# Kernel tuning notes

Measured on AMD Instinct MI355X. Metric: run time of the kernel, lower is better.

Reference implementation:

```python
import jax, jax.numpy as jnp
import numpy as np

B, S, D = 2, 2048, 2048
NH, NKV, HD = 32, 8, 64
RATIO = NH // NKV  # 4
EPS = 1e-6


def setup_inputs() -> dict:
    key = jax.random.key(0)
    ks = jax.random.split(key, 6)
    x = jax.random.normal(ks[0], (B, S, D), dtype=jnp.float32)
    # weights stored (in, out) so projection is x @ W
    wq = jax.random.normal(ks[1], (D, NH * HD), dtype=jnp.float32) * 0.02
    wk = jax.random.normal(ks[2], (D, NKV * HD), dtype=jnp.float32) * 0.02
    wv = jax.random.normal(ks[3], (D, NKV * HD), dtype=jnp.float32) * 0.02
    wo = jax.random.normal(ks[4], (NH * HD, D), dtype=jnp.float32) * 0.02
    q_scale = jnp.ones((HD,), dtype=jnp.float32)
    k_scale = jnp.ones((HD,), dtype=jnp.float32)
    # RoPE tables (S, HD): duplicated-half layout
    inv_freq = 1.0 / (10000.0 ** (np.arange(0, HD, 2, dtype=np.float32) / HD))
    t = np.arange(S, dtype=np.float32)
    freqs = np.outer(t, inv_freq)  # (S, HD/2)
    emb = np.concatenate([freqs, freqs], axis=-1)  # (S, HD)
    cos = jnp.asarray(np.cos(emb))
    sin = jnp.asarray(np.sin(emb))
    # causal mask: True above diagonal = masked
    mask = jnp.triu(jnp.ones((S, S), dtype=jnp.bool_), k=1)
    return {"x": x, "wq": wq, "wk": wk, "wv": wv, "wo": wo,
            "q_scale": q_scale, "k_scale": k_scale,
            "cos": cos, "sin": sin, "mask": mask}


def _rms_norm(x, scale):
    # Qwen3-compatible: compute in fp32, cast back
    idt = x.dtype
    xf = x.astype(jnp.float32)
    nx = xf * jax.lax.rsqrt(jnp.mean(xf * xf, axis=-1, keepdims=True) + EPS)
    return (nx * scale).astype(idt)


def _rope(x, cos, sin):
    # x: (b, h, s, hd); cos/sin: (s, hd)
    hd = x.shape[-1]
    x1, x2 = x[..., : hd // 2], x[..., hd // 2:]
    rot = jnp.concatenate([-x2, x1], axis=-1)
    return x * cos[None, None] + rot * sin[None, None]


def reference(x, wq, wk, wv, wo, q_scale, k_scale, cos, sin, mask):
    b, sl, _ = x.shape
    q = (x @ wq).reshape(b, sl, NH, HD).transpose(0, 2, 1, 3)    # (b, nh, s, hd)
    k = (x @ wk).reshape(b, sl, NKV, HD).transpose(0, 2, 1, 3)   # (b, nkv, s, hd)
    v = (x @ wv).reshape(b, sl, NKV, HD).transpose(0, 2, 1, 3)   # (b, nkv, s, hd)
    q = _rms_norm(q, q_scale)
    k = _rms_norm(k, k_scale)
    q = _rope(q, cos, sin)
    k = _rope(k, cos, sin)
    # GQA: repeat KV heads
    k = jnp.repeat(k, RATIO, axis=1)  # (b, nh, s, hd)
    v = jnp.repeat(v, RATIO, axis=1)
    scores = jnp.einsum('bhqd,bhkd->bhqk', q, k) / jnp.sqrt(jnp.float32(HD))
    scores = jnp.where(mask[None, None], jnp.finfo(scores.dtype).min, scores)
    attn = jax.nn.softmax(scores, axis=-1)
    out = jnp.einsum('bhqk,bhkd->bhqd', attn, v)
    out = out.transpose(0, 2, 1, 3).reshape(b, sl, NH * HD)
    return out @ wo
```

## Files before the change

### kernel.cpp

```cpp
#include <hip/hip_runtime.h>
#include <hip/hip_bf16.h>

typedef float f32x4 __attribute__((ext_vector_type(4)));
typedef float f32x16 __attribute__((ext_vector_type(16)));
typedef short s16x8 __attribute__((ext_vector_type(8)));
typedef unsigned short u16;
typedef unsigned short u16x8 __attribute__((ext_vector_type(8)));
typedef unsigned short u16x4 __attribute__((ext_vector_type(4)));
typedef unsigned int u32;
typedef unsigned int u32x4 __attribute__((ext_vector_type(4)));

#define MROWS 4096
#define NQKV  3072
#define DMODEL 2048

#define EXP2(x) __builtin_amdgcn_exp2f(x)

__device__ __forceinline__ u16 f2bf(float f) {
  __hip_bfloat16 h = __float2bfloat16(f);
  return __builtin_bit_cast(u16, h);
}
__device__ __forceinline__ float bf2f(u16 u) {
  __hip_bfloat16 h = __builtin_bit_cast(__hip_bfloat16, u);
  return __bfloat162float(h);
}

typedef __attribute__((address_space(3))) unsigned int lds_u32_t;
typedef const __attribute__((address_space(1))) unsigned int glb_u32_t;
__device__ __forceinline__ void gload_lds16(const void* g, void* l) {
  __builtin_amdgcn_global_load_lds((glb_u32_t*)g, (lds_u32_t*)l, 16, 0, 0);
}

__global__ __launch_bounds__(256) void k_conv_x(const float* __restrict__ x, u16* __restrict__ o) {
  size_t i = ((size_t)blockIdx.x * 256 + threadIdx.x) * 4;
  float4 v = *(const float4*)(x + i);
  u16x4 r = { f2bf(v.x), f2bf(v.y), f2bf(v.z), f2bf(v.w) };
  *(u16x4*)(o + i) = r;
}

__global__ __launch_bounds__(256) void k_transw(const float* __restrict__ src, u16* __restrict__ dst,
                                                int N, int K) {
  __shared__ u16 t[64][68];
  int n0 = blockIdx.x * 64, k0 = blockIdx.y * 64;
  int tid = threadIdx.x;
#pragma unroll
  for (int r = 0; r < 4; ++r) {
    int k = r * 16 + (tid >> 4);
    int n = (tid & 15) * 4;
    float4 v = *(const float4*)(src + (size_t)(k0 + k) * N + n0 + n);
    t[n + 0][k] = f2bf(v.x);
    t[n + 1][k] = f2bf(v.y);
    t[n + 2][k] = f2bf(v.z);
    t[n + 3][k] = f2bf(v.w);
  }
  __syncthreads();
#pragma unroll
  for (int r = 0; r < 4; ++r) {
    int n = r * 16 + (tid >> 4);
    int k = (tid & 15) * 4;
    u16x4 o = { t[n][k], t[n][k + 1], t[n][k + 2], t[n][k + 3] };
    *(u16x4*)(dst + (size_t)(n0 + n) * K + k0 + k) = o;
  }
}

template <int BM, int BN, typename OutT>
__global__ __launch_bounds__(512, 2)
void k_gemm8(const u16* __restrict__ A, const u16* __restrict__ Bt,
             OutT* __restrict__ C, int M, int N, int K, int nbx) {
  static_assert(BM == 128, "A staging assumes one full 512x16B round");
  constexpr int WM = 2, WN = 4;
  constexpr int MF = BM / 16 / WM;
  constexpr int NF = BN / 16 / WN;
  __shared__ u16 sA[2][2][BM][32];
  __shared__ u16 sB[2][2][BN][32];
  const int nwg = gridDim.x;
  const int chunk = nwg >> 3;
  const int wg = (blockIdx.x & 7) * chunk + (blockIdx.x >> 3);
  const int m0 = (wg / nbx) * BM, n0 = (wg % nbx) * BN;
  const int tid = threadIdx.x;
  const int l = tid & 63;
  const int lo = l & 15, hi = l >> 4;
  const int wid = tid >> 6;
  const int wm = wid >> 2, wn = wid & 3;
  const int nkt = K >> 6;

  f32x4 acc[MF][NF] = {};

  auto STAGE = [&](int buf, int ks, int t) {
    {
      const int D = tid * 16;
      const int row = D >> 6;
      const int srcb = (D & 63) ^ (((row >> 1) & 3) << 4);
      gload_lds16((const char*)(A + (size_t)(m0 + row) * K + t * 64 + ks * 32) + srcb,
                  (char*)(&sA[buf][ks][0][0]) + D);
    }
#pragma unroll
    for (int i = 0; i < 2; ++i) {
      const int u = i * 512 + tid;
      if ((BN * 4) % 512 == 0 || u < BN * 4) {
        const int D = u * 16;
        const int row = D >> 6;
        const int srcb = (D & 63) ^ (((row >> 1) & 3) << 4);
        gload_lds16((const char*)(Bt + (size_t)(n0 + row) * K + t * 64 + ks * 32) + srcb,
                    (char*)(&sB[buf][ks][0][0]) + D);
      }
    }
  };

  auto WAITVM = [&]() {
    if constexpr (BN == 192) {
      if (wid < 4) asm volatile("s_waitcnt vmcnt(3)" ::: "memory");
      else         asm volatile("s_waitcnt vmcnt(2)" ::: "memory");
    } else {
      asm volatile("s_waitcnt vmcnt(3)" ::: "memory");
    }
  };

  auto PHASE = [&](int buf, int ks, int t1, bool st, int vmmode) {
    s16x8 a[MF], b[NF];
#pragma unroll
    for (int mf = 0; mf < MF; ++mf) {
      const int row = wm * (MF * 16) + mf * 16 + lo;
      a[mf] = *(const s16x8*)((const char*)(&sA[buf][ks][0][0]) + row * 64 +
                              ((hi * 16) ^ (((row >> 1) & 3) << 4)));
    }
#pragma unroll
    for (int nf = 0; nf < NF; ++nf) {
      const int row = wn * (NF * 16) + nf * 16 + lo;
      b[nf] = *(const s16x8*)((const char*)(&sB[buf][ks][0][0]) + row * 64 +
                              ((hi * 16) ^ (((row >> 1) & 3) << 4)));
    }
    if (st) STAGE(buf ^ 1, ks, t1);
    __builtin_amdgcn_sched_barrier(0);
    __builtin_amdgcn_s_barrier();
    asm volatile("s_waitcnt lgkmcnt(0)" ::: "memory");
    __builtin_amdgcn_sched_barrier(0);
    __builtin_amdgcn_s_setprio(1);
#pragma unroll
    for (int mf = 0; mf < MF; ++mf)
#pragma unroll
      for (int nf = 0; nf < NF; ++nf)
        acc[mf][nf] = __builtin_amdgcn_mfma_f32_16x16x32_bf16(a[mf], b[nf], acc[mf][nf], 0, 0, 0);
    __builtin_amdgcn_s_setprio(0);
    if (vmmode == 1) WAITVM();
    else if (vmmode == 2) asm volatile("s_waitcnt vmcnt(0)" ::: "memory");
    __builtin_amdgcn_sched_barrier(0);
    __builtin_amdgcn_s_barrier();
  };

  STAGE(0, 0, 0);
  STAGE(0, 1, 0);
  WAITVM();
  __builtin_amdgcn_s_barrier();

  for (int t = 0; t < nkt; ++t) {
    const int buf = t & 1;
    const bool st = (t + 1 < nkt);
    PHASE(buf, 0, t + 1, st, st ? 1 : 2);
    PHASE(buf, 1, t + 1, st, st ? 1 : 0);
  }

#pragma unroll
  for (int mf = 0; mf < MF; ++mf)
#pragma unroll
    for (int nf = 0; nf < NF; ++nf)
#pragma unroll
      for (int r = 0; r < 4; ++r) {
        const int row = m0 + wm * (MF * 16) + mf * 16 + hi * 4 + r;
        const int col = n0 + wn * (NF * 16) + nf * 16 + lo;
        if constexpr (__is_same(OutT, float)) C[(size_t)row * N + col] = acc[mf][nf][r];
        else                                  C[(size_t)row * N + col] = f2bf(acc[mf][nf][r]);
      }
}

__global__ __launch_bounds__(256) void k_normrope(const u16* __restrict__ qkv, u16* __restrict__ qn,
                                                  u16* __restrict__ kn, const float* __restrict__ qs,
                                                  const float* __restrict__ ksc,
                                                  const float* __restrict__ cosb,
                                                  const float* __restrict__ sinb) {
  int j = blockIdx.x * 4 + (threadIdx.x >> 6);
  int l = threadIdx.x & 63;
  bool isQ = j < MROWS * 32;
  int m, head, incol;
  if (isQ) { m = j >> 5; head = j & 31; incol = head * 64; }
  else     { int j2 = j - MROWS * 32; m = j2 >> 3; head = j2 & 7; incol = 2048 + head * 64; }
  float v = bf2f(qkv[(size_t)m * NQKV + incol + l]);
  float ss = v * v;
#pragma unroll
  for (int off = 1; off < 64; off <<= 1) ss += __shfl_xor(ss, off, 64);
  float inv = rsqrtf(ss * (1.0f / 64.0f) + 1e-6f);
  float nx = v * inv * (isQ ? qs[l] : ksc[l]);
  int s = m & 2047;
  float c = cosb[s * 64 + l], sn = sinb[s * 64 + l];
  float partner = __shfl_xor(nx, 32, 64);
  float rot = (l < 32) ? -partner : partner;
  float outv = nx * c + rot * sn;
  if (isQ) {
    outv *= 0.125f * 1.44269504088896f;
    qn[(size_t)m * 2048 + incol + l] = f2bf(outv);
  } else {
    kn[(size_t)m * 512 + head * 64 + l] = f2bf(outv);
  }
}

__global__ __launch_bounds__(256) void k_vtrans(const u16* __restrict__ qkv, u16* __restrict__ vt) {
  __shared__ u16 t[64][68];
  int s0 = blockIdx.x * 64;
  int bk = blockIdx.y;
  int tid = threadIdx.x;
#pragma unroll
  for (int r = 0; r < 4; ++r) {
    int s = r * 16 + (tid >> 4);
    int d = (tid & 15) * 4;
    u16x4 v = *(const u16x4*)(qkv + (size_t)((bk >> 3) * 2048 + s0 + s) * NQKV + 2560 + (bk & 7) * 64 + d);
    t[d + 0][s] = v[0];
    t[d + 1][s] = v[1];
    t[d + 2][s] = v[2];
    t[d + 3][s] = v[3];
  }
  __syncthreads();
#pragma unroll
  for (int r = 0; r < 4; ++r) {
    int d = r * 16 + (tid >> 4);
    int sl = (tid & 15) * 4;
    u16x4 o = { t[d][sl], t[d][sl + 1], t[d][sl + 2], t[d][sl + 3] };
    *(u16x4*)(vt + (size_t)(bk * 64 + d) * 2048 + s0 + sl) = o;
  }
}

__global__ __launch_bounds__(256) void k_attn(const u16* __restrict__ qn, const u16* __restrict__ kn,
                                              const u16* __restrict__ vt, u16* __restrict__ aout) {
  __shared__ char sK[2][64 * 128];
  __shared__ char sV[2][64 * 128];
  const int bid = blockIdx.x;
  const int xcd = bid & 7, jj = bid >> 3;
  const int bkv = xcd | ((jj & 1) << 3);
  const int hsub = (jj >> 1) & 3, p = jj >> 3;
  const int b = bkv >> 3, kvh = bkv & 7, h = kvh * 4 + hsub;
  const int tid = threadIdx.x, l = tid & 63, w = tid >> 6;
  const int l31 = l & 31, l5 = l >> 5;
  const int qtA = 15 - p, qtB = p;
  const int nA = 2 * qtA + 2;
  const u16* kbase = kn + (size_t)(b * 2048) * 512 + kvh * 64;
  const u16* vbase = vt + (size_t)((b * 8 + kvh) * 64) * 2048;
  const int srow = tid >> 3;
  const int scol = (tid & 7) * 8;

  u16x8 krg0, krg1, vrg0, vrg1;
  auto issue = [&](int kv0) {
    krg0 = *(const u16x8*)(kbase + (size_t)(kv0 + srow) * 512 + scol);
    krg1 = *(const u16x8*)(kbase + (size_t)(kv0 + srow + 32) * 512 + scol);
    vrg0 = *(const u16x8*)(vbase + (size_t)srow * 2048 + kv0 + scol);
    vrg1 = *(const u16x8*)(vbase + (size_t)(srow + 32) * 2048 + kv0 + scol);
  };
  auto stash = [&](int buf) {
    const int cb = scol * 2;
    const int r0 = srow, r1 = srow + 32;
    *(u16x8*)(sK[buf] + r0 * 128 + (cb ^ ((r0 & 7) << 4))) = krg0;
    *(u16x8*)(sK[buf] + r1 * 128 + (cb ^ ((r1 & 7) << 4))) = krg1;
    *(u16x8*)(sV[buf] + r0 * 128 + (cb ^ ((r0 & 7) << 4))) = vrg0;
    *(u16x8*)(sV[buf] + r1 * 128 + (cb ^ ((r1 & 7) << 4))) = vrg1;
  };

  s16x8 qf[4];
  f32x16 O0, O1;
  float mst, lst;
  auto loadQ = [&](int qt_) {
    const u16* qp = qn + (size_t)(b * 2048 + qt_ * 128 + w * 32 + l31) * 2048 + h * 64 + l5 * 8;
#pragma unroll
    for (int ki = 0; ki < 4; ++ki) qf[ki] = *(const s16x8*)(qp + ki * 16);
#pragma unroll
    for (int r = 0; r < 16; ++r) { O0[r] = 0.f; O1[r] = 0.f; }
    mst = -1e30f; lst = 0.f;
  };
  auto epi = [&](int qt_) {
    const float inv = 1.0f / lst;
    const size_t rowoff = (size_t)(b * 2048 + qt_ * 128 + w * 32 + l31) * 2048 + h * 64;
#pragma unroll
    for (int g = 0; g < 4; ++g) {
      const int d0 = 8 * g + 4 * l5;
      u16x4 o0 = { f2bf(O0[4*g+0]*inv), f2bf(O0[4*g+1]*inv), f2bf(O0[4*g+2]*inv), f2bf(O0[4*g+3]*inv) };
      *(u16x4*)(aout + rowoff + d0) = o0;
      u16x4 o1 = { f2bf(O1[4*g+0]*inv), f2bf(O1[4*g+1]*inv), f2bf(O1[4*g+2]*inv), f2bf(O1[4*g+3]*inv) };
      *(u16x4*)(aout + rowoff + 32 + d0) = o1;
    }
  };

  loadQ(qtA);
  issue(0);
  stash(0);
  for (int s = 0; s < 34; ++s) {
    const int cur = s & 1;
    __syncthreads();
    const int qt = (s < nA) ? qtA : qtB;
    const int kvt = (s < nA) ? s : s - nA;
    if (s + 1 < 34) {
      const int kn2 = (s + 1 < nA) ? s + 1 : s + 1 - nA;
      issue(kn2 * 64);
    }
    f32x16 sc0, sc1;
#pragma unroll
    for (int r = 0; r < 16; ++r) { sc0[r] = 0.f; sc1[r] = 0.f; }
#pragma unroll
    for (int ki = 0; ki < 4; ++ki) {
      const int cb = ki * 32 + l5 * 16;
      const int r0 = l31, r1 = 32 + l31;
      s16x8 a0 = *(const s16x8*)(sK[cur] + r0 * 128 + (cb ^ ((r0 & 7) << 4)));
      s16x8 a1 = *(const s16x8*)(sK[cur] + r1 * 128 + (cb ^ ((r1 & 7) << 4)));
      sc0 = __builtin_amdgcn_mfma_f32_32x32x16_bf16(a0, qf[ki], sc0, 0, 0, 0);
      sc1 = __builtin_amdgcn_mfma_f32_32x32x16_bf16(a1, qf[ki], sc1, 0, 0, 0);
    }
    if (kvt >= 2 * qt) {
      const int qrow = qt * 128 + w * 32 + l31;
      const int kb0 = kvt * 64;
#pragma unroll
      for (int r = 0; r < 16; ++r) {
        const int krow = (r & 3) + 8 * (r >> 2) + 4 * l5;
        if (kb0 + krow > qrow) sc0[r] = -1e30f;
        if (kb0 + 32 + krow > qrow) sc1[r] = -1e30f;
      }
    }
    float mA = sc0[0], mB = sc0[1], mC = sc0[2], mD = sc0[3];
#pragma unroll
    for (int r = 4; r < 16; r += 4) {
      mA = fmaxf(mA, sc0[r]); mB = fmaxf(mB, sc0[r+1]);
      mC = fmaxf(mC, sc0[r+2]); mD = fmaxf(mD, sc0[r+3]);
    }
#pragma unroll
    for (int r = 0; r < 16; r += 4) {
      mA = fmaxf(mA, sc1[r]); mB = fmaxf(mB, sc1[r+1]);
      mC = fmaxf(mC, sc1[r+2]); mD = fmaxf(mD, sc1[r+3]);
    }
    float mloc = fmaxf(fmaxf(mA, mB), fmaxf(mC, mD));
    mloc = fmaxf(mloc, __shfl_xor(mloc, 32, 64));
    if (!__all(mloc <= mst + 8.0f)) {
      const float mnew = fmaxf(mst, mloc);
      const float alpha = EXP2(mst - mnew);
      mst = mnew;
      lst *= alpha;
#pragma unroll
      for (int r = 0; r < 16; ++r) { O0[r] *= alpha; O1[r] *= alpha; }
    }
    float rs = 0.f;
    u32 pk0[4][2], pk1[4][2];
#pragma unroll
    for (int g = 0; g < 4; ++g) {
      float a0 = EXP2(sc0[4*g+0] - mst), a1 = EXP2(sc0[4*g+1] - mst);
      float a2 = EXP2(sc0[4*g+2] - mst), a3 = EXP2(sc0[4*g+3] - mst);
      float b0 = EXP2(sc1[4*g+0] - mst), b1 = EXP2(sc1[4*g+1] - mst);
      float b2 = EXP2(sc1[4*g+2] - mst), b3 = EXP2(sc1[4*g+3] - mst);
      rs += ((a0 + a1) + (a2 + a3)) + ((b0 + b1) + (b2 + b3));
      pk0[g][0] = (u32)f2bf(a0) | ((u32)f2bf(a1) << 16);
      pk0[g][1] = (u32)f2bf(a2) | ((u32)f2bf(a3) << 16);
      pk1[g][0] = (u32)f2bf(b0) | ((u32)f2bf(b1) << 16);
      pk1[g][1] = (u32)f2bf(b2) | ((u32)f2bf(b3) << 16);
    }
    rs += __shfl_xor(rs, 32, 64);
    lst += rs;
#define PV_STEP(PK, H2, KB)                                                   \
    {                                                                         \
      u32 A0 = PK[2*(H2)][0], A1 = PK[2*(H2)][1];                             \
      u32 B0 = PK[2*(H2)+1][0], B1 = PK[2*(H2)+1][1];                         \
      u32 s0 = l5 ? A0 : B0, s1 = l5 ? A1 : B1;                               \
      u32 rc0 = (u32)__shfl_xor((int)s0, 32, 64);                             \
      u32 rc1 = (u32)__shfl_xor((int)s1, 32, 64);                             \
      u32 w0 = l5 ? rc0 : A0, w1 = l5 ? rc1 : A1;                             \
      u32 w2 = l5 ? B0 : rc0, w3 = l5 ? B1 : rc1;                             \
      u32x4 wv_ = { w0, w1, w2, w3 };                                         \
      s16x8 pb = __builtin_bit_cast(s16x8, wv_);                              \
      const int cb = (KB) * 32 + l5 * 16;                                     \
      const int rv0 = l31, rv1 = 32 + l31;                                    \
      s16x8 v0 = *(const s16x8*)(sV[cur] + rv0 * 128 + (cb ^ ((rv0 & 7) << 4))); \
      s16x8 v1 = *(const s16x8*)(sV[cur] + rv1 * 128 + (cb ^ ((rv1 & 7) << 4))); \
      O0 = __builtin_amdgcn_mfma_f32_32x32x16_bf16(v0, pb, O0, 0, 0, 0);      \
      O1 = __builtin_amdgcn_mfma_f32_32x32x16_bf16(v1, pb, O1, 0, 0, 0);      \
    }
    PV_STEP(pk0, 0, 0)
    PV_STEP(pk0, 1, 1)
    PV_STEP(pk1, 0, 2)
    PV_STEP(pk1, 1, 3)
#undef PV_STEP
    if (s + 1 < 34) stash(cur ^ 1);
    if (s == nA - 1) { epi(qtA); loadQ(qtB); }
    else if (s == 33) epi(qtB);
  }
}

extern "C" void kernel_launch(void* const* d_in, const int* in_sizes, int n_in,
                              void* d_out, int out_size, void* d_ws, size_t ws_size,
                              hipStream_t stream) {
  (void)in_sizes; (void)n_in; (void)out_size; (void)ws_size;
  const float* x    = (const float*)d_in[0];
  const float* wq   = (const float*)d_in[1];
  const float* wk   = (const float*)d_in[2];
  const float* wv   = (const float*)d_in[3];
  const float* wo   = (const float*)d_in[4];
  const float* qs   = (const float*)d_in[5];
  const float* ksc  = (const float*)d_in[6];
  const float* cosb = (const float*)d_in[7];
  const float* sinb = (const float*)d_in[8];
  float* out = (float*)d_out;
  char* ws = (char*)d_ws;
  u16* xbf   = (u16*)(ws);
  u16* wqkvt = (u16*)(ws + 16777216);
  u16* wot   = (u16*)(ws + 29360128);
  u16* qkv   = (u16*)(ws + 37748736);
  u16* qn    = (u16*)(ws + 62914560);
  u16* kn    = (u16*)(ws + 79691776);
  u16* vt    = (u16*)(ws + 83886080);
  u16* aout  = (u16*)(ws + 88080384);

  k_conv_x<<<8192, 256, 0, stream>>>(x, xbf);
  k_transw<<<dim3(32, 32), 256, 0, stream>>>(wq, wqkvt, 2048, 2048);
  k_transw<<<dim3(8, 32), 256, 0, stream>>>(wk, wqkvt + (size_t)2048 * 2048, 512, 2048);
  k_transw<<<dim3(8, 32), 256, 0, stream>>>(wv, wqkvt + (size_t)2560 * 2048, 512, 2048);
  k_transw<<<dim3(32, 32), 256, 0, stream>>>(wo, wot, 2048, 2048);
  k_gemm8<128, 192, u16><<<512, 512, 0, stream>>>(xbf, wqkvt, qkv, MROWS, NQKV, 2048, 16);
  k_normrope<<<40960, 256, 0, stream>>>(qkv, qn, kn, qs, ksc, cosb, sinb);
  k_vtrans<<<dim3(32, 16), 256, 0, stream>>>(qkv, vt);
  k_attn<<<512, 256, 0, stream>>>(qn, kn, vt, aout);
  k_gemm8<128, 256, float><<<256, 512, 0, stream>>>(aout, wot, out, MROWS, DMODEL, 2048, 8);
}
```

Measured before the change: 228.3 us.

## Split paired causal q-tiles into separate blocks and add MFMA priority hints

The attention kernel used to run two complementary query tiles (15-p and p) in one block so every block did the same 34 KV steps. Now each block handles a single query tile, giving 1024 blocks with variable loop lengths ordered longest-first so the hardware scheduler can balance load. It also raises wave priority around the MFMA sections with s_setprio. This adds parallelism and removes the mid-loop epilogue and Q reload, but makes block runtimes uneven and loses the XCD-aware block-to-head mapping.

```diff
diff --git a/kernel.cpp b/kernel.cpp
--- a/kernel.cpp
+++ b/kernel.cpp
@@ -233,14 +233,16 @@
   __shared__ char sK[2][64 * 128];
   __shared__ char sV[2][64 * 128];
   const int bid = blockIdx.x;
-  const int xcd = bid & 7, jj = bid >> 3;
-  const int bkv = xcd | ((jj & 1) << 3);
-  const int hsub = (jj >> 1) & 3, p = jj >> 3;
-  const int b = bkv >> 3, kvh = bkv & 7, h = kvh * 4 + hsub;
+  const int kvh = bid & 7;
+  const int b = (bid >> 3) & 1;
+  const int hsub = (bid >> 4) & 3;
+  const int a = (bid >> 6) & 3;
+  const int k = bid >> 8;
+  const int qt = (k == 0) ? 15 - a : (k == 1) ? 8 + a : (k == 2) ? 7 - a : a;
+  const int h = kvh * 4 + hsub;
   const int tid = threadIdx.x, l = tid & 63, w = tid >> 6;
   const int l31 = l & 31, l5 = l >> 5;
-  const int qtA = 15 - p, qtB = p;
-  const int nA = 2 * qtA + 2;
+  const int nkv = 2 * qt + 2;
   const u16* kbase = kn + (size_t)(b * 2048) * 512 + kvh * 64;
   const u16* vbase = vt + (size_t)((b * 8 + kvh) * 64) * 2048;
   const int srow = tid >> 3;
@@ -264,43 +266,25 @@
 
   s16x8 qf[4];
   f32x16 O0, O1;
-  float mst, lst;
-  auto loadQ = [&](int qt_) {
-    const u16* qp = qn + (size_t)(b * 2048 + qt_ * 128 + w * 32 + l31) * 2048 + h * 64 + l5 * 8;
+  float mst = -1e30f, lst = 0.f;
+  {
+    const u16* qp = qn + (size_t)(b * 2048 + qt * 128 + w * 32 + l31) * 2048 + h * 64 + l5 * 8;
 #pragma unroll
     for (int ki = 0; ki < 4; ++ki) qf[ki] = *(const s16x8*)(qp + ki * 16);
 #pragma unroll
     for (int r = 0; r < 16; ++r) { O0[r] = 0.f; O1[r] = 0.f; }
-    mst = -1e30f; lst = 0.f;
-  };
-  auto epi = [&](int qt_) {
-    const float inv = 1.0f / lst;
-    const size_t rowoff = (size_t)(b * 2048 + qt_ * 128 + w * 32 + l31) * 2048 + h * 64;
-#pragma unroll
-    for (int g = 0; g < 4; ++g) {
-      const int d0 = 8 * g + 4 * l5;
-      u16x4 o0 = { f2bf(O0[4*g+0]*inv), f2bf(O0[4*g+1]*inv), f2bf(O0[4*g+2]*inv), f2bf(O0[4*g+3]*inv) };
-      *(u16x4*)(aout + rowoff + d0) = o0;
-      u16x4 o1 = { f2bf(O1[4*g+0]*inv), f2bf(O1[4*g+1]*inv), f2bf(O1[4*g+2]*inv), f2bf(O1[4*g+3]*inv) };
-      *(u16x4*)(aout + rowoff + 32 + d0) = o1;
-    }
-  };
-
-  loadQ(qtA);
+  }
+
   issue(0);
   stash(0);
-  for (int s = 0; s < 34; ++s) {
+  for (int s = 0; s < nkv; ++s) {
     const int cur = s & 1;
     __syncthreads();
-    const int qt = (s < nA) ? qtA : qtB;
-    const int kvt = (s < nA) ? s : s - nA;
-    if (s + 1 < 34) {
-      const int kn2 = (s + 1 < nA) ? s + 1 : s + 1 - nA;
-      issue(kn2 * 64);
-    }
+    if (s + 1 < nkv) issue((s + 1) * 64);
     f32x16 sc0, sc1;
 #pragma unroll
     for (int r = 0; r < 16; ++r) { sc0[r] = 0.f; sc1[r] = 0.f; }
+    __builtin_amdgcn_s_setprio(1);
 #pragma unroll
     for (int ki = 0; ki < 4; ++ki) {
       const int cb = ki * 32 + l5 * 16;
@@ -310,9 +294,10 @@
       sc0 = __builtin_amdgcn_mfma_f32_32x32x16_bf16(a0, qf[ki], sc0, 0, 0, 0);
       sc1 = __builtin_amdgcn_mfma_f32_32x32x16_bf16(a1, qf[ki], sc1, 0, 0, 0);
     }
-    if (kvt >= 2 * qt) {
+    __builtin_amdgcn_s_setprio(0);
+    if (s >= 2 * qt) {
       const int qrow = qt * 128 + w * 32 + l31;
-      const int kb0 = kvt * 64;
+      const int kb0 = s * 64;
 #pragma unroll
       for (int r = 0; r < 16; ++r) {
         const int krow = (r & 3) + 8 * (r >> 2) + 4 * l5;
@@ -372,17 +357,29 @@
       const int rv0 = l31, rv1 = 32 + l31;                                    \
       s16x8 v0 = *(const s16x8*)(sV[cur] + rv0 * 128 + (cb ^ ((rv0 & 7) << 4))); \
       s16x8 v1 = *(const s16x8*)(sV[cur] + rv1 * 128 + (cb ^ ((rv1 & 7) << 4))); \
+      __builtin_amdgcn_s_setprio(1);                                          \
       O0 = __builtin_amdgcn_mfma_f32_32x32x16_bf16(v0, pb, O0, 0, 0, 0);      \
       O1 = __builtin_amdgcn_mfma_f32_32x32x16_bf16(v1, pb, O1, 0, 0, 0);      \
+      __builtin_amdgcn_s_setprio(0);                                          \
     }
     PV_STEP(pk0, 0, 0)
     PV_STEP(pk0, 1, 1)
     PV_STEP(pk1, 0, 2)
     PV_STEP(pk1, 1, 3)
 #undef PV_STEP
-    if (s + 1 < 34) stash(cur ^ 1);
-    if (s == nA - 1) { epi(qtA); loadQ(qtB); }
-    else if (s == 33) epi(qtB);
+    if (s + 1 < nkv) stash(cur ^ 1);
+  }
+  {
+    const float inv = 1.0f / lst;
+    const size_t rowoff = (size_t)(b * 2048 + qt * 128 + w * 32 + l31) * 2048 + h * 64;
+#pragma unroll
+    for (int g = 0; g < 4; ++g) {
+      const int d0 = 8 * g + 4 * l5;
+      u16x4 o0 = { f2bf(O0[4*g+0]*inv), f2bf(O0[4*g+1]*inv), f2bf(O0[4*g+2]*inv), f2bf(O0[4*g+3]*inv) };
+      *(u16x4*)(aout + rowoff + d0) = o0;
+      u16x4 o1 = { f2bf(O1[4*g+0]*inv), f2bf(O1[4*g+1]*inv), f2bf(O1[4*g+2]*inv), f2bf(O1[4*g+3]*inv) };
+      *(u16x4*)(aout + rowoff + 32 + d0) = o1;
+    }
   }
 }
 
@@ -418,6 +415,6 @@
   k_gemm8<128, 192, u16><<<512, 512, 0, stream>>>(xbf, wqkvt, qkv, MROWS, NQKV, 2048, 16);
   k_normrope<<<40960, 256, 0, stream>>>(qkv, qn, kn, qs, ksc, cosb, sinb);
   k_vtrans<<<dim3(32, 16), 256, 0, stream>>>(qkv, vt);
-  k_attn<<<512, 256, 0, stream>>>(qn, kn, vt, aout);
+  k_attn<<<1024, 256, 0, stream>>>(qn, kn, vt, aout);
   k_gemm8<128, 256, float><<<256, 512, 0, stream>>>(aout, wot, out, MROWS, DMODEL, 2048, 8);
 }
```

After: 223.2 us. 2.2% less time.
